# Kernel tuning notes

Measured on AMD Instinct MI355X. Metric: run time of the kernel, lower is better.

## Reference

```python
import jax, jax.numpy as jnp
import numpy as np

D_MODEL = 1024
D_FF = 8192
N_ELEM = 64            # d2 (elements per block)
D1 = D_FF // N_ELEM    # 128 block rows
BATCH = 2048


def setup_inputs() -> dict:
    key = jax.random.key(0)
    k1, k2, k3, k4, k5 = jax.random.split(key, 5)
    # xavier-uniform-like init for w1 (d_model, d_ff) -> view (d_model, d1, d2)
    bound1 = float(np.sqrt(6.0 / (D_MODEL + D_FF)))
    w1 = jax.random.uniform(k1, (D_MODEL, D1, N_ELEM), jnp.float32, -bound1, bound1)
    # w2 (d_ff, d_model) -> view (d2, d1, d_model); kernel_scaling=True multiplies by sqrt(d2)
    w2 = jax.random.uniform(k2, (N_ELEM, D1, D_MODEL), jnp.float32, -bound1, bound1)
    w2 = w2 * (N_ELEM ** 0.5)
    b2 = jax.random.normal(k3, (D_MODEL,), jnp.float32)
    x = jax.random.normal(k4, (BATCH, D_MODEL), jnp.float32)
    quant_mask = jax.random.randint(k5, (BATCH, D1), 0, N_ELEM, jnp.int32)
    return {"quant_mask": quant_mask, "x": x, "w1": w1, "w2": w2, "b2": b2}


def reference(quant_mask, x, w1, w2, b2):
    # predict-mode path of SparseFFMain (multiply_by_controller_output=False)
    d1 = w1.shape[1]
    w1p = jnp.transpose(w1, (1, 2, 0))   # (d1, d2, d_model)
    w2p = jnp.transpose(w2, (1, 0, 2))   # (d1, d2, d_model)
    rows = jnp.arange(d1)[None, :]        # (1, d1) broadcasts over batch
    # per-sample gathered expert sub-blocks: (B, d1, d_model)
    w = w1p[rows, quant_mask]
    v = w2p[rows, quant_mask]
    mid = jnp.einsum('bd,bjd->bj', x, w)   # (B, d1)
    relu = jax.nn.relu(mid)
    res = jnp.einsum('bj,bjd->bd', relu, v) + b2  # (B, d_model)
    return (quant_mask, res)
```

## Files before the change

kernel.cpp:

```cpp
#include <hip/hip_runtime.h>

#define D_MODEL 1024
#define D_FF    8192
#define N_ELEM  64
#define D1      128
#define BATCH   2048
#define B_T     8
#define NJT     8
#define JT      16

typedef unsigned short u16;
typedef unsigned int   u32;
typedef _Float16 h2    __attribute__((ext_vector_type(2)));
typedef float    f32x4 __attribute__((ext_vector_type(4)));
typedef u32      u32x2 __attribute__((ext_vector_type(2)));
typedef u32      u32x4 __attribute__((ext_vector_type(4)));

__device__ __forceinline__ h2 as_h2(u32 u) { union { u32 i; h2 h; } c; c.i = u; return c.h; }
__device__ __forceinline__ u32 pkh(float a, float b) {
    union { h2 h; u32 u; } c; c.h.x = (_Float16)a; c.h.y = (_Float16)b; return c.u;
}
__device__ __forceinline__ u16 f2h(float f) {
    union { _Float16 h; u16 u; } c; c.h = (_Float16)f; return c.u;
}
__device__ __forceinline__ f32x4 ntload4(const float* p) {
    return __builtin_nontemporal_load((const f32x4*)p);
}
__device__ __forceinline__ float dot2(u32 a, u32 b, float c) {
#if __has_builtin(__builtin_amdgcn_fdot2)
    return __builtin_amdgcn_fdot2(as_h2(a), as_h2(b), c, false);
#else
    const h2 ha = as_h2(a), hb = as_h2(b);
    c = fmaf((float)ha.x, (float)hb.x, c);
    return fmaf((float)ha.y, (float)hb.y, c);
#endif
}
__device__ __forceinline__ float dot8(uint4 w, uint4 q, float c) {
    c = dot2(w.x, q.x, c);
    c = dot2(w.y, q.y, c);
    c = dot2(w.z, q.z, c);
    c = dot2(w.w, q.w, c);
    return c;
}

#if __has_builtin(__builtin_amdgcn_update_dpp)
#define WRITER_LANE 63
#define DPP_ADD(x, ctrl)                                                      \
    x += __builtin_bit_cast(float, __builtin_amdgcn_update_dpp(               \
        0, __builtin_bit_cast(int, x), ctrl, 0xf, 0xf, true))
__device__ __forceinline__ float wave_sum64(float x) {
    DPP_ADD(x, 0x111);
    DPP_ADD(x, 0x112);
    DPP_ADD(x, 0x114);
    DPP_ADD(x, 0x118);
    DPP_ADD(x, 0x142);
    DPP_ADD(x, 0x143);
    return x;
}
#else
#define WRITER_LANE 0
__device__ __forceinline__ float wave_sum64(float x) {
#pragma unroll
    for (int off = 32; off; off >>= 1) x += __shfl_down(x, off);
    return x;
}
#endif
__device__ __forceinline__ float bcast_lane(float x, int srclane) {
#if __has_builtin(__builtin_amdgcn_readlane)
    return __builtin_bit_cast(float,
        __builtin_amdgcn_readlane(__builtin_bit_cast(int, x), srclane));
#else
    return __shfl(x, srclane);
#endif
}

#define TW1_BLOCKS ((D_FF / 64) * (D_MODEL / 64))
__global__ __launch_bounds__(256) void prep_weights(const float* __restrict__ w1,
                                                    u16* __restrict__ w1h,
                                                    const float* __restrict__ w2,
                                                    u16* __restrict__ w2h) {
    __shared__ float tile[64][65];
    if (blockIdx.x < TW1_BLOCKS) {
        const int c0 = (blockIdx.x & (D_FF / 64 - 1)) * 64;
        const int d0 = (blockIdx.x >> 7) * 64;
        const int tx = threadIdx.x & 15;
        const int ty = threadIdx.x >> 4;
#pragma unroll
        for (int r = 0; r < 4; ++r) {
            const int row = ty * 4 + r;
            const float4 v = *(const float4*)(w1 + (size_t)(d0 + row) * D_FF + c0 + tx * 4);
            tile[row][tx * 4 + 0] = v.x;
            tile[row][tx * 4 + 1] = v.y;
            tile[row][tx * 4 + 2] = v.z;
            tile[row][tx * 4 + 3] = v.w;
        }
        __syncthreads();
#pragma unroll
        for (int r = 0; r < 4; ++r) {
            const int c = ty * 4 + r;
            ushort4 o;
            o.x = f2h(tile[tx * 4 + 0][c]);
            o.y = f2h(tile[tx * 4 + 1][c]);
            o.z = f2h(tile[tx * 4 + 2][c]);
            o.w = f2h(tile[tx * 4 + 3][c]);
            *(ushort4*)(w1h + (size_t)(c0 + c) * D_MODEL + d0 + tx * 4) = o;
        }
    } else {
        const size_t i = ((size_t)(blockIdx.x - TW1_BLOCKS) * 256 + threadIdx.x) * 8;
        const float4 a = *(const float4*)(w2 + i);
        const float4 b = *(const float4*)(w2 + i + 4);
        ushort4 oa, ob;
        oa.x = f2h(a.x); oa.y = f2h(a.y); oa.z = f2h(a.z); oa.w = f2h(a.w);
        ob.x = f2h(b.x); ob.y = f2h(b.y); ob.z = f2h(b.z); ob.w = f2h(b.w);
        *(ushort4*)(w2h + i)     = oa;
        *(ushort4*)(w2h + i + 4) = ob;
    }
}

__global__ __launch_bounds__(256) void sparse_ff_jt(const int* __restrict__ mask,
                                                    const float* __restrict__ x,
                                                    const u16* __restrict__ w1h_,
                                                    const u16* __restrict__ w2h_,
                                                    u16* __restrict__ part) {
    const _Float16* w1h = (const _Float16*)w1h_;
    const _Float16* w2h = (const _Float16*)w2h_;
    __shared__ u16 x_lds[B_T][D_MODEL];
    __shared__ int m_lds[B_T][JT];

    const int jt = blockIdx.x & (NJT - 1);
    const int b0 = (blockIdx.x >> 3) * B_T;
    const int t = threadIdx.x;
    const int wave = t >> 6;
    const int lane = t & 63;

#pragma unroll
    for (int r = 0; r < B_T; ++r) {
        const f32x4 v = ntload4(x + (size_t)(b0 + r) * D_MODEL + t * 4);
        u32x2 o; o.x = pkh(v.x, v.y); o.y = pkh(v.z, v.w);
        *(u32x2*)&x_lds[r][t * 4] = o;
    }
    if (t < B_T * JT) {
        m_lds[t >> 4][t & 15] = mask[(b0 + (t >> 4)) * D1 + jt * JT + (t & 15)];
    }
    __syncthreads();

#pragma unroll
    for (int rep = 0; rep < 2; ++rep) {
        const int bi = wave * 2 + rep;
        const uint4 xA = *(const uint4*)&x_lds[bi][lane * 8];
        const uint4 xB = *(const uint4*)&x_lds[bi][512 + lane * 8];

        int   mj[JT];
        float rj[JT];

#pragma unroll
        for (int jj = 0; jj < JT; jj += 4) {
            mj[jj + 0] = m_lds[bi][jj + 0];
            mj[jj + 1] = m_lds[bi][jj + 1];
            mj[jj + 2] = m_lds[bi][jj + 2];
            mj[jj + 3] = m_lds[bi][jj + 3];
            const int j0 = jt * JT + jj;
            const _Float16* c0 = w1h + (size_t)(((j0 + 0) << 6) + mj[jj + 0]) * D_MODEL + lane * 8;
            const _Float16* c1 = w1h + (size_t)(((j0 + 1) << 6) + mj[jj + 1]) * D_MODEL + lane * 8;
            const _Float16* c2 = w1h + (size_t)(((j0 + 2) << 6) + mj[jj + 2]) * D_MODEL + lane * 8;
            const _Float16* c3 = w1h + (size_t)(((j0 + 3) << 6) + mj[jj + 3]) * D_MODEL + lane * 8;
            const uint4 a0 = *(const uint4*)c0;
            const uint4 a1 = *(const uint4*)c1;
            const uint4 a2 = *(const uint4*)c2;
            const uint4 a3 = *(const uint4*)c3;
            const uint4 e0 = *(const uint4*)(c0 + 512);
            const uint4 e1 = *(const uint4*)(c1 + 512);
            const uint4 e2 = *(const uint4*)(c2 + 512);
            const uint4 e3 = *(const uint4*)(c3 + 512);

            float s0 = dot8(a0, xA, 0.f); s0 = dot8(e0, xB, s0);
            float s1 = dot8(a1, xA, 0.f); s1 = dot8(e1, xB, s1);
            float s2 = dot8(a2, xA, 0.f); s2 = dot8(e2, xB, s2);
            float s3 = dot8(a3, xA, 0.f); s3 = dot8(e3, xB, s3);

            s0 = wave_sum64(s0);
            s1 = wave_sum64(s1);
            s2 = wave_sum64(s2);
            s3 = wave_sum64(s3);
            rj[jj + 0] = fmaxf(bcast_lane(s0, WRITER_LANE), 0.f);
            rj[jj + 1] = fmaxf(bcast_lane(s1, WRITER_LANE), 0.f);
            rj[jj + 2] = fmaxf(bcast_lane(s2, WRITER_LANE), 0.f);
            rj[jj + 3] = fmaxf(bcast_lane(s3, WRITER_LANE), 0.f);
        }

        float c0 = 0.f, c1 = 0.f, c2 = 0.f, c3 = 0.f;
        float c4 = 0.f, c5 = 0.f, c6 = 0.f, c7 = 0.f;
        float c8 = 0.f, c9 = 0.f, cA = 0.f, cB = 0.f;
        float cC = 0.f, cD = 0.f, cE = 0.f, cF = 0.f;
#pragma unroll
        for (int jj = 0; jj < JT; ++jj) {
            const float r = rj[jj];
            const _Float16* row = w2h
                + (size_t)(mj[jj] * D1 + jt * JT + jj) * D_MODEL + lane * 16;
            const uint4 v0 = *(const uint4*)row;
            const uint4 v1 = *(const uint4*)(row + 8);
            const h2 q0 = as_h2(v0.x), q1 = as_h2(v0.y);
            const h2 q2 = as_h2(v0.z), q3 = as_h2(v0.w);
            const h2 q4 = as_h2(v1.x), q5 = as_h2(v1.y);
            const h2 q6 = as_h2(v1.z), q7 = as_h2(v1.w);
            c0 = fmaf(r, (float)q0.x, c0); c1 = fmaf(r, (float)q0.y, c1);
            c2 = fmaf(r, (float)q1.x, c2); c3 = fmaf(r, (float)q1.y, c3);
            c4 = fmaf(r, (float)q2.x, c4); c5 = fmaf(r, (float)q2.y, c5);
            c6 = fmaf(r, (float)q3.x, c6); c7 = fmaf(r, (float)q3.y, c7);
            c8 = fmaf(r, (float)q4.x, c8); c9 = fmaf(r, (float)q4.y, c9);
            cA = fmaf(r, (float)q5.x, cA); cB = fmaf(r, (float)q5.y, cB);
            cC = fmaf(r, (float)q6.x, cC); cD = fmaf(r, (float)q6.y, cD);
            cE = fmaf(r, (float)q7.x, cE); cF = fmaf(r, (float)q7.y, cF);
        }
        u32x4 oA, oB;
        oA.x = pkh(c0, c1); oA.y = pkh(c2, c3);
        oA.z = pkh(c4, c5); oA.w = pkh(c6, c7);
        oB.x = pkh(c8, c9); oB.y = pkh(cA, cB);
        oB.z = pkh(cC, cD); oB.w = pkh(cE, cF);
        u16* pp = part + ((size_t)jt * BATCH + (b0 + bi)) * D_MODEL + lane * 16;
        __builtin_nontemporal_store(oA, (u32x4*)pp);
        __builtin_nontemporal_store(oB, (u32x4*)(pp + 8));
    }
}

__global__ __launch_bounds__(256) void reduce_partials(const int* __restrict__ mask,
                                                       const float* __restrict__ b2,
                                                       const u16* __restrict__ part,
                                                       float* __restrict__ out) {
    const int b = blockIdx.x;
    const int t = threadIdx.x;
    if (t < D1) out[(size_t)b * D1 + t] = (float)mask[b * D1 + t];

    const int d0 = t * 4;
    const float4 bv = *(const float4*)(b2 + d0);
    float a0 = bv.x, a1 = bv.y, a2 = bv.z, a3 = bv.w;
#pragma unroll
    for (int jt = 0; jt < NJT; ++jt) {
        const uint2 v = *(const uint2*)(part + ((size_t)jt * BATCH + b) * D_MODEL + d0);
        const h2 p0 = as_h2(v.x), p1 = as_h2(v.y);
        a0 += (float)p0.x; a1 += (float)p0.y;
        a2 += (float)p1.x; a3 += (float)p1.y;
    }
    *(float4*)(out + (size_t)BATCH * D1 + (size_t)b * D_MODEL + d0) =
        make_float4(a0, a1, a2, a3);
}

__global__ __launch_bounds__(256) void sparse_ff_f32_raw(const int* __restrict__ mask,
                                                         const float* __restrict__ x,
                                                         const float* __restrict__ w1,
                                                         const float* __restrict__ w2,
                                                         const float* __restrict__ b2,
                                                         float* __restrict__ out) {
    __shared__ float x_lds[D_MODEL];
    __shared__ float relu_lds[D1];
    __shared__ int   m_lds[D1];
    const int b = blockIdx.x, t = threadIdx.x;
    const int wave = t >> 6, lane = t & 63;
    *(float4*)&x_lds[t * 4] = *(const float4*)(x + (size_t)b * D_MODEL + t * 4);
    if (t < D1) {
        const int mv = mask[b * D1 + t];
        m_lds[t] = mv;
        out[(size_t)b * D1 + t] = (float)mv;
    }
    __syncthreads();
    for (int jj = 0; jj < 32; ++jj) {
        const int j = wave * 32 + jj;
        const int m = m_lds[j];
        float acc = 0.f;
#pragma unroll
        for (int c = 0; c < 16; ++c) {
            const int d = c * 64 + lane;
            acc = fmaf(w1[(size_t)d * D_FF + j * N_ELEM + m], x_lds[d], acc);
        }
#pragma unroll
        for (int off = 32; off; off >>= 1) acc += __shfl_down(acc, off);
        if (lane == 0) relu_lds[j] = fmaxf(acc, 0.f);
    }
    __syncthreads();
    const int dm0 = t * 4;
    const float4 bv = *(const float4*)(b2 + dm0);
    float a0 = bv.x, a1 = bv.y, a2 = bv.z, a3 = bv.w;
    for (int j = 0; j < D1; ++j) {
        const float r = relu_lds[j];
        if (r > 0.f) {
            const float4 wv = *(const float4*)(w2 + (size_t)(m_lds[j] * D1 + j) * D_MODEL + dm0);
            a0 = fmaf(r, wv.x, a0); a1 = fmaf(r, wv.y, a1);
            a2 = fmaf(r, wv.z, a2); a3 = fmaf(r, wv.w, a3);
        }
    }
    *(float4*)(out + (size_t)BATCH * D1 + (size_t)b * D_MODEL + dm0) =
        make_float4(a0, a1, a2, a3);
}

extern "C" void kernel_launch(void* const* d_in, const int* in_sizes, int n_in,
                              void* d_out, int out_size, void* d_ws, size_t ws_size,
                              hipStream_t stream) {
    const int*   mask = (const int*)d_in[0];
    const float* x    = (const float*)d_in[1];
    const float* w1   = (const float*)d_in[2];
    const float* w2   = (const float*)d_in[3];
    const float* b2   = (const float*)d_in[4];
    float* out = (float*)d_out;

    const size_t w1h_bytes  = (size_t)D_FF * D_MODEL * sizeof(u16);
    const size_t w2h_bytes  = (size_t)D_FF * D_MODEL * sizeof(u16);
    const size_t part_bytes = (size_t)NJT * BATCH * D_MODEL * sizeof(u16);

    if (ws_size >= w1h_bytes + w2h_bytes + part_bytes) {
        u16* w1h  = (u16*)d_ws;
        u16* w2h  = (u16*)((char*)d_ws + w1h_bytes);
        u16* part = (u16*)((char*)d_ws + w1h_bytes + w2h_bytes);
        const int cast_blocks = (D_FF * D_MODEL / 8) / 256;
        prep_weights<<<TW1_BLOCKS + cast_blocks, 256, 0, stream>>>(w1, w1h, w2, w2h);
        sparse_ff_jt<<<(BATCH / B_T) * NJT, 256, 0, stream>>>(mask, x, w1h, w2h, part);
        reduce_partials<<<BATCH, 256, 0, stream>>>(mask, b2, part, out);
    } else {
        sparse_ff_f32_raw<<<BATCH, 256, 0, stream>>>(mask, x, w1, w2, b2, out);
    }
}
```

Before: 193.8 us.

## Drop LDS staging and interleave W1/W2 passes to cut registers

Removes the shared-memory staging of x and mask and the block-wide barrier, so each wave loads its own x row directly from global memory and reads mask indices inline. The two-phase loop (all 16 W1 dot products, then all 16 W2 accumulations) becomes a single loop over pairs of j that does the dot product and the W2 accumulation together, so the mj/rj arrays no longer need to be held in registers. A launch bound of 8 blocks per SM is added to push for higher occupancy. The cost is fewer independent loads in flight per iteration (2 instead of 4), which may expose more memory latency.

```diff
diff --git a/kernel.cpp b/kernel.cpp
--- a/kernel.cpp
+++ b/kernel.cpp
@@ -117,107 +117,104 @@
     }
 }
 
-__global__ __launch_bounds__(256) void sparse_ff_jt(const int* __restrict__ mask,
-                                                    const float* __restrict__ x,
-                                                    const u16* __restrict__ w1h_,
-                                                    const u16* __restrict__ w2h_,
-                                                    u16* __restrict__ part) {
+__global__ __launch_bounds__(256, 8) void sparse_ff_jt(const int* __restrict__ mask,
+                                                       const float* __restrict__ x,
+                                                       const u16* __restrict__ w1h_,
+                                                       const u16* __restrict__ w2h_,
+                                                       u16* __restrict__ part) {
     const _Float16* w1h = (const _Float16*)w1h_;
     const _Float16* w2h = (const _Float16*)w2h_;
-    __shared__ u16 x_lds[B_T][D_MODEL];
-    __shared__ int m_lds[B_T][JT];
 
     const int jt = blockIdx.x & (NJT - 1);
     const int b0 = (blockIdx.x >> 3) * B_T;
-    const int t = threadIdx.x;
-    const int wave = t >> 6;
-    const int lane = t & 63;
-
-#pragma unroll
-    for (int r = 0; r < B_T; ++r) {
-        const f32x4 v = ntload4(x + (size_t)(b0 + r) * D_MODEL + t * 4);
-        u32x2 o; o.x = pkh(v.x, v.y); o.y = pkh(v.z, v.w);
-        *(u32x2*)&x_lds[r][t * 4] = o;
-    }
-    if (t < B_T * JT) {
-        m_lds[t >> 4][t & 15] = mask[(b0 + (t >> 4)) * D1 + jt * JT + (t & 15)];
-    }
-    __syncthreads();
+    const int wave = threadIdx.x >> 6;
+    const int lane = threadIdx.x & 63;
 
 #pragma unroll
     for (int rep = 0; rep < 2; ++rep) {
         const int bi = wave * 2 + rep;
-        const uint4 xA = *(const uint4*)&x_lds[bi][lane * 8];
-        const uint4 xB = *(const uint4*)&x_lds[bi][512 + lane * 8];
-
-        int   mj[JT];
-        float rj[JT];
-
-#pragma unroll
-        for (int jj = 0; jj < JT; jj += 4) {
-            mj[jj + 0] = m_lds[bi][jj + 0];
-            mj[jj + 1] = m_lds[bi][jj + 1];
-            mj[jj + 2] = m_lds[bi][jj + 2];
-            mj[jj + 3] = m_lds[bi][jj + 3];
-            const int j0 = jt * JT + jj;
-            const _Float16* c0 = w1h + (size_t)(((j0 + 0) << 6) + mj[jj + 0]) * D_MODEL + lane * 8;
-            const _Float16* c1 = w1h + (size_t)(((j0 + 1) << 6) + mj[jj + 1]) * D_MODEL + lane * 8;
-            const _Float16* c2 = w1h + (size_t)(((j0 + 2) << 6) + mj[jj + 2]) * D_MODEL + lane * 8;
-            const _Float16* c3 = w1h + (size_t)(((j0 + 3) << 6) + mj[jj + 3]) * D_MODEL + lane * 8;
-            const uint4 a0 = *(const uint4*)c0;
-            const uint4 a1 = *(const uint4*)c1;
-            const uint4 a2 = *(const uint4*)c2;
-            const uint4 a3 = *(const uint4*)c3;
-            const uint4 e0 = *(const uint4*)(c0 + 512);
-            const uint4 e1 = *(const uint4*)(c1 + 512);
-            const uint4 e2 = *(const uint4*)(c2 + 512);
-            const uint4 e3 = *(const uint4*)(c3 + 512);
-
-            float s0 = dot8(a0, xA, 0.f); s0 = dot8(e0, xB, s0);
-            float s1 = dot8(a1, xA, 0.f); s1 = dot8(e1, xB, s1);
-            float s2 = dot8(a2, xA, 0.f); s2 = dot8(e2, xB, s2);
-            float s3 = dot8(a3, xA, 0.f); s3 = dot8(e3, xB, s3);
-
-            s0 = wave_sum64(s0);
-            s1 = wave_sum64(s1);
-            s2 = wave_sum64(s2);
-            s3 = wave_sum64(s3);
-            rj[jj + 0] = fmaxf(bcast_lane(s0, WRITER_LANE), 0.f);
-            rj[jj + 1] = fmaxf(bcast_lane(s1, WRITER_LANE), 0.f);
-            rj[jj + 2] = fmaxf(bcast_lane(s2, WRITER_LANE), 0.f);
-            rj[jj + 3] = fmaxf(bcast_lane(s3, WRITER_LANE), 0.f);
-        }
+        const int brow = b0 + bi;
+
+        const float* xr = x + (size_t)brow * D_MODEL;
+        const f32x4 x0 = ntload4(xr + lane * 8);
+        const f32x4 x1 = ntload4(xr + lane * 8 + 4);
+        const f32x4 x2 = ntload4(xr + 512 + lane * 8);
+        const f32x4 x3 = ntload4(xr + 512 + lane * 8 + 4);
+        uint4 xA, xB;
+        xA.x = pkh(x0.x, x0.y); xA.y = pkh(x0.z, x0.w);
+        xA.z = pkh(x1.x, x1.y); xA.w = pkh(x1.z, x1.w);
+        xB.x = pkh(x2.x, x2.y); xB.y = pkh(x2.z, x2.w);
+        xB.z = pkh(x3.x, x3.y); xB.w = pkh(x3.z, x3.w);
 
         float c0 = 0.f, c1 = 0.f, c2 = 0.f, c3 = 0.f;
         float c4 = 0.f, c5 = 0.f, c6 = 0.f, c7 = 0.f;
         float c8 = 0.f, c9 = 0.f, cA = 0.f, cB = 0.f;
         float cC = 0.f, cD = 0.f, cE = 0.f, cF = 0.f;
-#pragma unroll
-        for (int jj = 0; jj < JT; ++jj) {
-            const float r = rj[jj];
-            const _Float16* row = w2h
-                + (size_t)(mj[jj] * D1 + jt * JT + jj) * D_MODEL + lane * 16;
-            const uint4 v0 = *(const uint4*)row;
-            const uint4 v1 = *(const uint4*)(row + 8);
-            const h2 q0 = as_h2(v0.x), q1 = as_h2(v0.y);
-            const h2 q2 = as_h2(v0.z), q3 = as_h2(v0.w);
-            const h2 q4 = as_h2(v1.x), q5 = as_h2(v1.y);
-            const h2 q6 = as_h2(v1.z), q7 = as_h2(v1.w);
-            c0 = fmaf(r, (float)q0.x, c0); c1 = fmaf(r, (float)q0.y, c1);
-            c2 = fmaf(r, (float)q1.x, c2); c3 = fmaf(r, (float)q1.y, c3);
-            c4 = fmaf(r, (float)q2.x, c4); c5 = fmaf(r, (float)q2.y, c5);
-            c6 = fmaf(r, (float)q3.x, c6); c7 = fmaf(r, (float)q3.y, c7);
-            c8 = fmaf(r, (float)q4.x, c8); c9 = fmaf(r, (float)q4.y, c9);
-            cA = fmaf(r, (float)q5.x, cA); cB = fmaf(r, (float)q5.y, cB);
-            cC = fmaf(r, (float)q6.x, cC); cD = fmaf(r, (float)q6.y, cD);
-            cE = fmaf(r, (float)q7.x, cE); cF = fmaf(r, (float)q7.y, cF);
-        }
+
+        const int mbase = brow * D1 + jt * JT;
+
+#pragma unroll
+        for (int jj = 0; jj < JT; jj += 2) {
+            const int m0 = mask[mbase + jj];
+            const int m1 = mask[mbase + jj + 1];
+            const int j0 = jt * JT + jj;
+
+            const _Float16* r0 = w1h + (size_t)(((j0 + 0) << 6) + m0) * D_MODEL + lane * 8;
+            const _Float16* r1 = w1h + (size_t)(((j0 + 1) << 6) + m1) * D_MODEL + lane * 8;
+            const uint4 a0 = *(const uint4*)r0;
+            const uint4 e0 = *(const uint4*)(r0 + 512);
+            const uint4 a1 = *(const uint4*)r1;
+            const uint4 e1 = *(const uint4*)(r1 + 512);
+
+            float s0 = dot8(a0, xA, 0.f); s0 = dot8(e0, xB, s0);
+            float s1 = dot8(a1, xA, 0.f); s1 = dot8(e1, xB, s1);
+            s0 = wave_sum64(s0);
+            s1 = wave_sum64(s1);
+            const float q0 = fmaxf(bcast_lane(s0, WRITER_LANE), 0.f);
+            const float q1 = fmaxf(bcast_lane(s1, WRITER_LANE), 0.f);
+
+            const _Float16* w0 = w2h + (size_t)(m0 * D1 + j0) * D_MODEL + lane * 16;
+            const _Float16* w1r = w2h + (size_t)(m1 * D1 + j0 + 1) * D_MODEL + lane * 16;
+            const uint4 va0 = *(const uint4*)w0;
+            const uint4 vb0 = *(const uint4*)(w0 + 8);
+            const uint4 va1 = *(const uint4*)w1r;
+            const uint4 vb1 = *(const uint4*)(w1r + 8);
+            {
+                const h2 p0 = as_h2(va0.x), p1 = as_h2(va0.y);
+                const h2 p2 = as_h2(va0.z), p3 = as_h2(va0.w);
+                const h2 p4 = as_h2(vb0.x), p5 = as_h2(vb0.y);
+                const h2 p6 = as_h2(vb0.z), p7 = as_h2(vb0.w);
+                c0 = fmaf(q0, (float)p0.x, c0); c1 = fmaf(q0, (float)p0.y, c1);
+                c2 = fmaf(q0, (float)p1.x, c2); c3 = fmaf(q0, (float)p1.y, c3);
+                c4 = fmaf(q0, (float)p2.x, c4); c5 = fmaf(q0, (float)p2.y, c5);
+                c6 = fmaf(q0, (float)p3.x, c6); c7 = fmaf(q0, (float)p3.y, c7);
+                c8 = fmaf(q0, (float)p4.x, c8); c9 = fmaf(q0, (float)p4.y, c9);
+                cA = fmaf(q0, (float)p5.x, cA); cB = fmaf(q0, (float)p5.y, cB);
+                cC = fmaf(q0, (float)p6.x, cC); cD = fmaf(q0, (float)p6.y, cD);
+                cE = fmaf(q0, (float)p7.x, cE); cF = fmaf(q0, (float)p7.y, cF);
+            }
+            {
+                const h2 p0 = as_h2(va1.x), p1 = as_h2(va1.y);
+                const h2 p2 = as_h2(va1.z), p3 = as_h2(va1.w);
+                const h2 p4 = as_h2(vb1.x), p5 = as_h2(vb1.y);
+                const h2 p6 = as_h2(vb1.z), p7 = as_h2(vb1.w);
+                c0 = fmaf(q1, (float)p0.x, c0); c1 = fmaf(q1, (float)p0.y, c1);
+                c2 = fmaf(q1, (float)p1.x, c2); c3 = fmaf(q1, (float)p1.y, c3);
+                c4 = fmaf(q1, (float)p2.x, c4); c5 = fmaf(q1, (float)p2.y, c5);
+                c6 = fmaf(q1, (float)p3.x, c6); c7 = fmaf(q1, (float)p3.y, c7);
+                c8 = fmaf(q1, (float)p4.x, c8); c9 = fmaf(q1, (float)p4.y, c9);
+                cA = fmaf(q1, (float)p5.x, cA); cB = fmaf(q1, (float)p5.y, cB);
+                cC = fmaf(q1, (float)p6.x, cC); cD = fmaf(q1, (float)p6.y, cD);
+                cE = fmaf(q1, (float)p7.x, cE); cF = fmaf(q1, (float)p7.y, cF);
+            }
+        }
+
         u32x4 oA, oB;
         oA.x = pkh(c0, c1); oA.y = pkh(c2, c3);
         oA.z = pkh(c4, c5); oA.w = pkh(c6, c7);
         oB.x = pkh(c8, c9); oB.y = pkh(cA, cB);
         oB.z = pkh(cC, cD); oB.w = pkh(cE, cF);
-        u16* pp = part + ((size_t)jt * BATCH + (b0 + bi)) * D_MODEL + lane * 16;
+        u16* pp = part + ((size_t)jt * BATCH + brow) * D_MODEL + lane * 16;
         __builtin_nontemporal_store(oA, (u32x4*)pp);
         __builtin_nontemporal_store(oB, (u32x4*)(pp + 8));
     }
```

After: 370.7 us. +91.3%, slower.
